# Kernel tuning notes

Hardware: AMD Instinct MI355X
Metric: run time of the kernel (lower is better)

## Reference

```python
import jax, jax.numpy as jnp
import numpy as np

N_NODES = 50000   # field_size == number of graph nodes
N_EDGES = 800000  # avg degree 16
VOCAB = 200000    # feature_size
EMB = 64          # embedding_size == in_dim
HID = 64          # num_hidden
SLOPE = 0.2       # leaky relu negative slope


def setup_inputs() -> dict:
    key = jax.random.key(0)
    ks = jax.random.split(key, 20)
    s = 0.05
    d = {}
    d["features"] = jax.random.randint(ks[0], (8, N_NODES), 0, VOCAB, dtype=jnp.int32)
    d["feature_values"] = jax.random.uniform(ks[1], (8, N_NODES), dtype=jnp.float32)
    d["src"] = jax.random.randint(ks[2], (N_EDGES,), 0, N_NODES, dtype=jnp.int32)
    d["dst"] = jax.random.randint(ks[3], (N_EDGES,), 0, N_NODES, dtype=jnp.int32)
    d["emb"] = jax.random.normal(ks[4], (VOCAB, EMB), jnp.float32) * s
    # layer 0: in=64 -> heads=2, out=64 (no residual)
    d["W0"]  = jax.random.normal(ks[5], (EMB, 2 * HID), jnp.float32) * s
    d["al0"] = jax.random.normal(ks[6], (2, HID), jnp.float32) * s
    d["ar0"] = jax.random.normal(ks[7], (2, HID), jnp.float32) * s
    d["b0"]  = jnp.zeros((2 * HID,), jnp.float32)
    # layer 1: in=128 -> heads=2, out=64 (identity residual since in == heads*out)
    d["W1"]  = jax.random.normal(ks[8], (2 * HID, 2 * HID), jnp.float32) * s
    d["al1"] = jax.random.normal(ks[9], (2, HID), jnp.float32) * s
    d["ar1"] = jax.random.normal(ks[10], (2, HID), jnp.float32) * s
    d["b1"]  = jnp.zeros((2 * HID,), jnp.float32)
    # output layer: in=128 -> heads=1, out=64 (projected residual), no activation
    d["W2"]    = jax.random.normal(ks[11], (2 * HID, EMB), jnp.float32) * s
    d["al2"]   = jax.random.normal(ks[12], (1, EMB), jnp.float32) * s
    d["ar2"]   = jax.random.normal(ks[13], (1, EMB), jnp.float32) * s
    d["b2"]    = jnp.zeros((EMB,), jnp.float32)
    d["resW2"] = jax.random.normal(ks[14], (2 * HID, EMB), jnp.float32) * s
    return d


def _gat_layer(h, src, dst, W, al, ar, b, res, act):
    """DGL-style GATConv. h: [N, in], W: [in, H*D], al/ar: [H, D]."""
    N = h.shape[0]
    H, D = al.shape
    fh = (h @ W).reshape(N, H, D)                      # [N, H, D]
    el = jnp.einsum('nhd,hd->nh', fh, al)              # [N, H]
    er = jnp.einsum('nhd,hd->nh', fh, ar)              # [N, H]
    e = jax.nn.leaky_relu(el[src] + er[dst], SLOPE)    # [E, H]
    # edge softmax grouped by destination node
    m = jax.ops.segment_max(e, dst, num_segments=N)
    m = jnp.where(jnp.isfinite(m), m, 0.0)
    ex = jnp.exp(e - m[dst])
    den = jax.ops.segment_sum(ex, dst, num_segments=N)
    alpha = ex / jnp.maximum(den[dst], 1e-9)           # [E, H]
    out = jax.ops.segment_sum(alpha[:, :, None] * fh[src], dst, num_segments=N)  # [N, H, D]
    if res is not None:
        out = out + res
    out = out + b.reshape(H, D)
    if act:
        out = jax.nn.elu(out)
    return out


def reference(features, feature_values, src, dst, emb,
              W0, al0, ar0, b0, W1, al1, ar1, b1,
              W2, al2, ar2, b2, resW2):
    # embedding lookup scaled by feature values: [B, field, emb]
    fe = emb[features] * feature_values[..., None]
    h = fe[0]                                          # [N_NODES, EMB]
    # layer 0: no residual, elu, flatten heads
    h = _gat_layer(h, src, dst, W0, al0, ar0, b0, None, True).reshape(N_NODES, -1)
    # layer 1: identity residual (in == heads*out), elu, flatten heads
    res1 = h.reshape(N_NODES, 2, HID)
    h = _gat_layer(h, src, dst, W1, al1, ar1, b1, res1, True).reshape(N_NODES, -1)
    # output layer: projected residual, no activation, mean over heads
    res2 = (h @ resW2).reshape(N_NODES, 1, EMB)
    logits = _gat_layer(h, src, dst, W2, al2, ar2, b2, res2, False).mean(axis=1)
    return logits
```

## Files before the change

kernel.cpp:

```cpp
#include <hip/hip_runtime.h>


typedef __attribute__((ext_vector_type(8))) short short8;
typedef __attribute__((ext_vector_type(4))) float float4v;

__device__ __forceinline__ float lrelu(float x){ return x >= 0.f ? x : 0.2f*x; }

__device__ __forceinline__ unsigned short f2bf(float f){
  unsigned int u = __float_as_uint(f);
  u += 0x7fffu + ((u >> 16) & 1u);
  return (unsigned short)(u >> 16);
}
__device__ __forceinline__ float bf2f(unsigned short u){
  return __uint_as_float((unsigned int)u << 16);
}
__device__ __forceinline__ float rl_f(float v, int l){
  return __int_as_float(__builtin_amdgcn_readlane(__float_as_int(v), l));
}

__global__ void k_zero_i32(int* __restrict__ p, int n){
  int i = blockIdx.x*blockDim.x + threadIdx.x;
  if (i < n) p[i] = 0;
}

__global__ void k_hist(const int* __restrict__ dst, int* __restrict__ counts, int E){
  int i = blockIdx.x*blockDim.x + threadIdx.x;
  if (i < E) atomicAdd(&counts[dst[i]], 1);
}

__global__ void k_scan_local(const int* __restrict__ counts, int* __restrict__ row_ptr,
                             int* __restrict__ bsum, int N){
  __shared__ int s[256];
  int t = threadIdx.x, g = blockIdx.x*256 + t;
  int v = (g < N) ? counts[g] : 0;
  s[t] = v; __syncthreads();
  #pragma unroll
  for (int off = 1; off < 256; off <<= 1){
    int x = 0;
    if (t >= off) x = s[t-off];
    __syncthreads();
    s[t] += x;
    __syncthreads();
  }
  if (g < N) row_ptr[g+1] = s[t];
  if (g == 0 && t == 0) row_ptr[0] = 0;
  if (t == 255) bsum[blockIdx.x] = s[255];
}

__global__ void k_scan_top(int* __restrict__ bsum, int nb){
  __shared__ int s[256];
  int t = threadIdx.x;
  int v = (t < nb) ? bsum[t] : 0;
  s[t] = v; __syncthreads();
  #pragma unroll
  for (int off = 1; off < 256; off <<= 1){
    int x = 0;
    if (t >= off) x = s[t-off];
    __syncthreads();
    s[t] += x;
    __syncthreads();
  }
  if (t < nb) bsum[t] = s[t] - v;
}

__global__ void k_scan_fix(int* __restrict__ row_ptr, const int* __restrict__ bsum, int N){
  int g = blockIdx.x*256 + threadIdx.x;
  if (g < N && blockIdx.x > 0) row_ptr[g+1] += bsum[blockIdx.x];
}

__global__ void k_scatter(const int* __restrict__ src, const int* __restrict__ dst,
                          const int* __restrict__ row_ptr, int* __restrict__ cursor,
                          int* __restrict__ ssrc, int E){
  int i = blockIdx.x*blockDim.x + threadIdx.x;
  if (i >= E) return;
  int d = dst[i];
  int pos = atomicAdd(&cursor[d], 1);
  ssrc[row_ptr[d] + pos] = src[i];
}

__global__ void k_wprep(const float* __restrict__ Wa, const float* __restrict__ Wb,
                        int IN, unsigned short* __restrict__ Wt){
  int id = blockIdx.x*256 + threadIdx.x;
  if (id >= 128*IN) return;
  int n = id / IN, k = id % IN;
  float v;
  if (Wb) v = (n < 64) ? Wa[k*64 + n] : Wb[k*64 + (n - 64)];
  else    v = Wa[k*128 + n];
  Wt[n*IN + k] = f2bf(v);
}

__global__ void k_embed(const int* __restrict__ feat, const float* __restrict__ fv,
                        const float* __restrict__ emb, unsigned int* __restrict__ h0b, int N){
  int t = blockIdx.x*blockDim.x + threadIdx.x;
  int n = t >> 4, c4 = t & 15;
  if (n >= N) return;
  float4 v = ((const float4*)(emb + (size_t)feat[n]*64))[c4];
  float sc = fv[n];
  unsigned int p0 = (unsigned)f2bf(v.x*sc) | ((unsigned)f2bf(v.y*sc) << 16);
  unsigned int p1 = (unsigned)f2bf(v.z*sc) | ((unsigned)f2bf(v.w*sc) << 16);
  h0b[(size_t)n*32 + c4*2]     = p0;
  h0b[(size_t)n*32 + c4*2 + 1] = p1;
}

template<int IN, int H>
__global__ __launch_bounds__(256) void k_gemm_mfma(
    const unsigned short* __restrict__ hb,
    const unsigned short* __restrict__ Wt,
    const float* __restrict__ al, const float* __restrict__ ar,
    unsigned short* __restrict__ fhb,
    float* __restrict__ elr, int N){
  constexpr int KS = IN/32;
  constexpr int LDP = IN + 8;
  __shared__ unsigned short Wt_s[128*LDP];
  const int t = threadIdx.x;
  const int lane = t & 63, wid = t >> 6;
  const int l15 = lane & 15, quad = lane >> 4;
  const int row0 = blockIdx.x*64 + wid*16;

  for (int id = t; id < 128*(IN/8); id += 256){
    int r = id/(IN/8), seg = id%(IN/8);
    ((uint4*)(Wt_s + r*LDP))[seg] = ((const uint4*)(Wt + (size_t)r*IN))[seg];
  }
  short8 a[KS];
  int arow = row0 + l15;
  #pragma unroll
  for (int s = 0; s < KS; s++){
    if (arow < N) a[s] = *(const short8*)(hb + (size_t)arow*IN + s*32 + quad*8);
    else          a[s] = short8{0,0,0,0,0,0,0,0};
  }
  __syncthreads();

  float4v acc[8];
  #pragma unroll
  for (int nt = 0; nt < 8; nt++) acc[nt] = float4v{0.f,0.f,0.f,0.f};
  #pragma unroll
  for (int nt = 0; nt < 8; nt++){
    #pragma unroll
    for (int s = 0; s < KS; s++){
      short8 b = *(const short8*)(Wt_s + (nt*16 + l15)*LDP + s*32 + quad*8);
      acc[nt] = __builtin_amdgcn_mfma_f32_16x16x32_bf16(a[s], b, acc[nt], 0, 0, 0);
    }
  }

  float alc[8], arc[8];
  #pragma unroll
  for (int nt = 0; nt < 8; nt++){
    bool hv = (H == 2) || (nt < 4);
    alc[nt] = hv ? al[nt*16 + l15] : 0.f;
    arc[nt] = hv ? ar[nt*16 + l15] : 0.f;
  }
  #pragma unroll
  for (int reg = 0; reg < 4; reg++){
    int row = row0 + quad*4 + reg;
    bool rv = row < N;
    if (rv){
      #pragma unroll
      for (int nt = 0; nt < 8; nt++)
        fhb[(size_t)row*128 + nt*16 + l15] = f2bf(acc[nt][reg]);
    }
    float pel0 = 0.f, per0 = 0.f, pel1 = 0.f, per1 = 0.f;
    #pragma unroll
    for (int nt = 0; nt < 4; nt++){
      pel0 += acc[nt][reg]*alc[nt];     per0 += acc[nt][reg]*arc[nt];
      pel1 += acc[nt+4][reg]*alc[nt+4]; per1 += acc[nt+4][reg]*arc[nt+4];
    }
    #pragma unroll
    for (int off = 1; off < 16; off <<= 1){
      pel0 += __shfl_xor(pel0, off, 64);
      pel1 += __shfl_xor(pel1, off, 64);
      per0 += __shfl_xor(per0, off, 64);
      per1 += __shfl_xor(per1, off, 64);
    }
    if (l15 == 0 && rv){
      elr[row*4+0] = pel0;
      elr[row*4+1] = (H == 2) ? pel1 : 0.f;
      elr[row*4+2] = per0;
      elr[row*4+3] = (H == 2) ? per1 : 0.f;
    }
  }
}

template<int H>
__global__ __launch_bounds__(256) void k_agg(
    const unsigned* __restrict__ fhb, const float* __restrict__ elr,
    const int* __restrict__ row_ptr, const int* __restrict__ ssrc,
    const float* __restrict__ bias, const float* __restrict__ res,
    int act, int res_from_fh,
    float* __restrict__ out, int out_ld, unsigned* __restrict__ outb, int N){
  int lane = threadIdx.x & 63, wid = threadIdx.x >> 6;
  int n = blockIdx.x*4 + wid;
  if (n >= N) return;
  int beg = row_ptr[n], end = row_ptr[n+1];
  float er0 = elr[n*4+2];
  float er1 = (H == 2) ? elr[n*4+3] : 0.f;

  float x0 = 0.f, x1 = 0.f;
  {
    int i = beg + lane;
    if (i < end){
      int s = ssrc[i];
      float2 el = *(const float2*)(elr + s*4);
      x0 = __expf(fminf(lrelu(el.x + er0), 30.f));
      if (H == 2) x1 = __expf(fminf(lrelu(el.y + er1), 30.f));
    }
  }
  float d0 = x0, d1 = x1;
  for (int i = beg + lane + 64; i < end; i += 64){
    int s = ssrc[i];
    float2 el = *(const float2*)(elr + s*4);
    d0 += __expf(fminf(lrelu(el.x + er0), 30.f));
    if (H == 2) d1 += __expf(fminf(lrelu(el.y + er1), 30.f));
  }
  #pragma unroll
  for (int off = 32; off >= 1; off >>= 1){
    d0 += __shfl_xor(d0, off, 64);
    if (H == 2) d1 += __shfl_xor(d1, off, 64);
  }
  float rd0 = d0 > 0.f ? 1.f/d0 : 0.f;
  float rd1 = (H == 2 && d1 > 0.f) ? 1.f/d1 : 0.f;

  float ax = 0.f, ay = 0.f;
  for (int base = beg; base < end; base += 64){
    int i = base + lane;
    int s = 0; float a0 = 0.f, a1 = 0.f;
    if (i < end){
      s = ssrc[i];
      if (base == beg){
        a0 = x0 * rd0; if (H == 2) a1 = x1 * rd1;
      } else {
        float2 el = *(const float2*)(elr + s*4);
        a0 = __expf(fminf(lrelu(el.x + er0), 30.f)) * rd0;
        if (H == 2) a1 = __expf(fminf(lrelu(el.y + er1), 30.f)) * rd1;
      }
    }
    int cnt  = min(64, end - base);
    int cnt8 = (cnt + 7) & ~7;
    if (H == 2){
      for (int j0 = 0; j0 < cnt8; j0 += 8){
        unsigned w[8]; float aj[8];
        #pragma unroll
        for (int u = 0; u < 8; u++){
          int sj = __builtin_amdgcn_readlane(s, j0 + u);
          w[u] = fhb[(size_t)sj*64 + lane];
        }
        #pragma unroll
        for (int u = 0; u < 8; u++){
          float aj0 = rl_f(a0, j0 + u);
          float aj1 = rl_f(a1, j0 + u);
          aj[u] = (lane < 32) ? aj0 : aj1;
        }
        #pragma unroll
        for (int u = 0; u < 8; u++){
          ax += bf2f((unsigned short)(w[u] & 0xffffu)) * aj[u];
          ay += bf2f((unsigned short)(w[u] >> 16))     * aj[u];
        }
      }
    } else {
      const unsigned short* fh16 = (const unsigned short*)fhb;
      for (int j0 = 0; j0 < cnt8; j0 += 8){
        unsigned short w[8]; float aj[8];
        #pragma unroll
        for (int u = 0; u < 8; u++){
          int sj = __builtin_amdgcn_readlane(s, j0 + u);
          w[u] = fh16[(size_t)sj*128 + lane];
        }
        #pragma unroll
        for (int u = 0; u < 8; u++) aj[u] = rl_f(a0, j0 + u);
        #pragma unroll
        for (int u = 0; u < 8; u++) ax += bf2f(w[u]) * aj[u];
      }
    }
  }
  if (H == 2){
    int c0 = lane*2;
    float o0 = ax + bias[c0], o1 = ay + bias[c0+1];
    if (res){ o0 += res[n*128 + c0]; o1 += res[n*128 + c0+1]; }
    if (act){ o0 = o0 > 0.f ? o0 : expm1f(o0); o1 = o1 > 0.f ? o1 : expm1f(o1); }
    *(float2*)(out + n*out_ld + c0) = make_float2(o0, o1);
    if (outb) outb[(size_t)n*64 + lane] = (unsigned)f2bf(o0) | ((unsigned)f2bf(o1) << 16);
  } else {
    const unsigned short* fh16 = (const unsigned short*)fhb;
    float o = ax + bias[lane];
    if (res_from_fh) o += bf2f(fh16[(size_t)n*128 + 64 + lane]);
    out[n*out_ld + lane] = o;
  }
}

extern "C" void kernel_launch(void* const* d_in, const int* in_sizes, int n_in,
                              void* d_out, int out_size, void* d_ws, size_t ws_size,
                              hipStream_t stream) {
  const int*   feat = (const int*)  d_in[0];
  const float* fv   = (const float*)d_in[1];
  const int*   src  = (const int*)  d_in[2];
  const int*   dst  = (const int*)  d_in[3];
  const float* emb  = (const float*)d_in[4];
  const float* W0   = (const float*)d_in[5];
  const float* al0  = (const float*)d_in[6];
  const float* ar0  = (const float*)d_in[7];
  const float* b0   = (const float*)d_in[8];
  const float* W1   = (const float*)d_in[9];
  const float* al1  = (const float*)d_in[10];
  const float* ar1  = (const float*)d_in[11];
  const float* b1   = (const float*)d_in[12];
  const float* W2   = (const float*)d_in[13];
  const float* al2  = (const float*)d_in[14];
  const float* ar2  = (const float*)d_in[15];
  const float* b2   = (const float*)d_in[16];
  const float* rW2  = (const float*)d_in[17];
  const int N = in_sizes[0] / 8;
  const int E = in_sizes[2];

  size_t off = 0;
  auto alloc = [&](size_t bytes) -> void* {
    void* p = (char*)d_ws + off;
    off = (off + bytes + 255) & ~(size_t)255;
    return p;
  };
  unsigned short* P1 = (unsigned short*)alloc((size_t)N*128*sizeof(unsigned short));
  float* P2     = (float*)alloc((size_t)N*128*sizeof(float));
  float* P3     = (float*)alloc((size_t)N*128*sizeof(float));
  unsigned short* hb = (unsigned short*)alloc((size_t)N*128*sizeof(unsigned short));
  float* elr    = (float*)alloc((size_t)N*4*sizeof(float));
  int* row_ptr  = (int*)alloc((size_t)(N+1)*sizeof(int));
  int* counts   = (int*)alloc((size_t)2*N*sizeof(int));
  int* cursor   = counts + N;
  int* ssrc     = (int*)alloc((size_t)E*sizeof(int));
  int* bsum     = (int*)alloc(256*sizeof(int));
  unsigned short* Wt0 = (unsigned short*)alloc((size_t)128*64*sizeof(unsigned short));
  unsigned short* Wt1 = (unsigned short*)alloc((size_t)128*128*sizeof(unsigned short));
  unsigned short* Wt2 = (unsigned short*)alloc((size_t)128*128*sizeof(unsigned short));

  int nb1 = (N + 255) / 256;
  k_zero_i32<<<(2*N + 255)/256, 256, 0, stream>>>(counts, 2*N);
  k_hist<<<(E + 255)/256, 256, 0, stream>>>(dst, counts, E);
  k_scan_local<<<nb1, 256, 0, stream>>>(counts, row_ptr, bsum, N);
  k_scan_top<<<1, 256, 0, stream>>>(bsum, nb1);
  k_scan_fix<<<nb1, 256, 0, stream>>>(row_ptr, bsum, N);
  k_scatter<<<(E + 255)/256, 256, 0, stream>>>(src, dst, row_ptr, cursor, ssrc, E);
  k_wprep<<<(128*64 + 255)/256, 256, 0, stream>>>(W0, nullptr, 64, Wt0);
  k_wprep<<<(128*128 + 255)/256, 256, 0, stream>>>(W1, nullptr, 128, Wt1);
  k_wprep<<<(128*128 + 255)/256, 256, 0, stream>>>(W2, rW2, 128, Wt2);
  k_embed<<<(N*16 + 255)/256, 256, 0, stream>>>(feat, fv, emb, (unsigned int*)hb, N);

  int gt = (N + 63)/64;
  int nagg = (N + 3)/4;
  k_gemm_mfma<64,2><<<gt, 256, 0, stream>>>(hb, Wt0, al0, ar0, P1, elr, N);
  k_agg<2><<<nagg, 256, 0, stream>>>((unsigned*)P1, elr, row_ptr, ssrc, b0, nullptr,
                                     1, 0, P2, 128, (unsigned*)hb, N);
  k_gemm_mfma<128,2><<<gt, 256, 0, stream>>>(hb, Wt1, al1, ar1, P1, elr, N);
  k_agg<2><<<nagg, 256, 0, stream>>>((unsigned*)P1, elr, row_ptr, ssrc, b1, P2,
                                     1, 0, P3, 128, (unsigned*)hb, N);
  k_gemm_mfma<128,1><<<gt, 256, 0, stream>>>(hb, Wt2, al2, ar2, P1, elr, N);
  k_agg<1><<<nagg, 256, 0, stream>>>((unsigned*)P1, elr, row_ptr, ssrc, b2, nullptr,
                                     0, 1, (float*)d_out, 64, nullptr, N);
}
```

Baseline: 367.4 us.

## Fuse embedding into first GEMM, merge weight prep, compress edge indices

Folds the embedding lookup and scaling into the first MFMA GEMM, so the bf16 h0 buffer is no longer written and read back. Merges the three weight-transpose launches into one kernel. Makes hist and scatter process 4 edges per thread, and stores sorted source indices as 16-bit to cut index traffic in aggregation. Raises the aggregation gather unroll from 8 to 16 for more loads in flight. The 16-bit indices only hold because N is 50000 (below 65536), so larger graphs would break.

```diff
diff --git a/kernel.cpp b/kernel.cpp
--- a/kernel.cpp
+++ b/kernel.cpp
@@ -24,8 +24,12 @@
 }
 
 __global__ void k_hist(const int* __restrict__ dst, int* __restrict__ counts, int E){
-  int i = blockIdx.x*blockDim.x + threadIdx.x;
-  if (i < E) atomicAdd(&counts[dst[i]], 1);
+  int i0 = (blockIdx.x*blockDim.x + threadIdx.x)*4;
+  #pragma unroll
+  for (int u = 0; u < 4; u++){
+    int i = i0 + u;
+    if (i < E) atomicAdd(&counts[dst[i]], 1);
+  }
 }
 
 __global__ void k_scan_local(const int* __restrict__ counts, int* __restrict__ row_ptr,
@@ -70,41 +74,41 @@
 
 __global__ void k_scatter(const int* __restrict__ src, const int* __restrict__ dst,
                           const int* __restrict__ row_ptr, int* __restrict__ cursor,
-                          int* __restrict__ ssrc, int E){
-  int i = blockIdx.x*blockDim.x + threadIdx.x;
-  if (i >= E) return;
-  int d = dst[i];
-  int pos = atomicAdd(&cursor[d], 1);
-  ssrc[row_ptr[d] + pos] = src[i];
-}
-
-__global__ void k_wprep(const float* __restrict__ Wa, const float* __restrict__ Wb,
-                        int IN, unsigned short* __restrict__ Wt){
+                          unsigned short* __restrict__ ssrc, int E){
+  int i0 = (blockIdx.x*blockDim.x + threadIdx.x)*4;
+  #pragma unroll
+  for (int u = 0; u < 4; u++){
+    int i = i0 + u;
+    if (i < E){
+      int d = dst[i];
+      int pos = atomicAdd(&cursor[d], 1);
+      ssrc[row_ptr[d] + pos] = (unsigned short)src[i];
+    }
+  }
+}
+
+__global__ void k_wprep_all(const float* __restrict__ W0, const float* __restrict__ W1,
+                            const float* __restrict__ W2, const float* __restrict__ rW2,
+                            unsigned short* __restrict__ Wt0, unsigned short* __restrict__ Wt1,
+                            unsigned short* __restrict__ Wt2){
   int id = blockIdx.x*256 + threadIdx.x;
-  if (id >= 128*IN) return;
-  int n = id / IN, k = id % IN;
-  float v;
-  if (Wb) v = (n < 64) ? Wa[k*64 + n] : Wb[k*64 + (n - 64)];
-  else    v = Wa[k*128 + n];
-  Wt[n*IN + k] = f2bf(v);
-}
-
-__global__ void k_embed(const int* __restrict__ feat, const float* __restrict__ fv,
-                        const float* __restrict__ emb, unsigned int* __restrict__ h0b, int N){
-  int t = blockIdx.x*blockDim.x + threadIdx.x;
-  int n = t >> 4, c4 = t & 15;
-  if (n >= N) return;
-  float4 v = ((const float4*)(emb + (size_t)feat[n]*64))[c4];
-  float sc = fv[n];
-  unsigned int p0 = (unsigned)f2bf(v.x*sc) | ((unsigned)f2bf(v.y*sc) << 16);
-  unsigned int p1 = (unsigned)f2bf(v.z*sc) | ((unsigned)f2bf(v.w*sc) << 16);
-  h0b[(size_t)n*32 + c4*2]     = p0;
-  h0b[(size_t)n*32 + c4*2 + 1] = p1;
-}
-
-template<int IN, int H>
+  if (id < 128*64){
+    int n = id/64, k = id%64;
+    Wt0[n*64 + k] = f2bf(W0[k*128 + n]);
+  } else if (id < 128*64 + 128*128){
+    int j = id - 128*64; int n = j/128, k = j%128;
+    Wt1[n*128 + k] = f2bf(W1[k*128 + n]);
+  } else if (id < 128*64 + 2*128*128){
+    int j = id - 128*64 - 128*128; int n = j/128, k = j%128;
+    float v = (n < 64) ? W2[k*64 + n] : rW2[k*64 + (n - 64)];
+    Wt2[n*128 + k] = f2bf(v);
+  }
+}
+
+template<int IN, int H, bool EMBED>
 __global__ __launch_bounds__(256) void k_gemm_mfma(
     const unsigned short* __restrict__ hb,
+    const int* __restrict__ feat, const float* __restrict__ fv, const float* __restrict__ emb,
     const unsigned short* __restrict__ Wt,
     const float* __restrict__ al, const float* __restrict__ ar,
     unsigned short* __restrict__ fhb,
@@ -123,10 +127,27 @@
   }
   short8 a[KS];
   int arow = row0 + l15;
-  #pragma unroll
-  for (int s = 0; s < KS; s++){
-    if (arow < N) a[s] = *(const short8*)(hb + (size_t)arow*IN + s*32 + quad*8);
-    else          a[s] = short8{0,0,0,0,0,0,0,0};
+  if (EMBED){
+    int f = 0; float sc = 0.f;
+    if (arow < N){ f = feat[arow]; sc = fv[arow]; }
+    #pragma unroll
+    for (int s = 0; s < KS; s++){
+      const float* ep = emb + (size_t)f*64 + s*32 + quad*8;
+      float4 v0 = ((const float4*)ep)[0];
+      float4 v1 = ((const float4*)ep)[1];
+      short8 av;
+      av[0]=(short)f2bf(v0.x*sc); av[1]=(short)f2bf(v0.y*sc);
+      av[2]=(short)f2bf(v0.z*sc); av[3]=(short)f2bf(v0.w*sc);
+      av[4]=(short)f2bf(v1.x*sc); av[5]=(short)f2bf(v1.y*sc);
+      av[6]=(short)f2bf(v1.z*sc); av[7]=(short)f2bf(v1.w*sc);
+      a[s] = av;
+    }
+  } else {
+    #pragma unroll
+    for (int s = 0; s < KS; s++){
+      if (arow < N) a[s] = *(const short8*)(hb + (size_t)arow*IN + s*32 + quad*8);
+      else          a[s] = short8{0,0,0,0,0,0,0,0};
+    }
   }
   __syncthreads();
 
@@ -183,7 +204,7 @@
 template<int H>
 __global__ __launch_bounds__(256) void k_agg(
     const unsigned* __restrict__ fhb, const float* __restrict__ elr,
-    const int* __restrict__ row_ptr, const int* __restrict__ ssrc,
+    const int* __restrict__ row_ptr, const unsigned short* __restrict__ ssrc,
     const float* __restrict__ bias, const float* __restrict__ res,
     int act, int res_from_fh,
     float* __restrict__ out, int out_ld, unsigned* __restrict__ outb, int N){
@@ -233,41 +254,41 @@
         if (H == 2) a1 = __expf(fminf(lrelu(el.y + er1), 30.f)) * rd1;
       }
     }
-    int cnt  = min(64, end - base);
-    int cnt8 = (cnt + 7) & ~7;
+    int cnt   = min(64, end - base);
+    int cnt16 = (cnt + 15) & ~15;
     if (H == 2){
-      for (int j0 = 0; j0 < cnt8; j0 += 8){
-        unsigned w[8]; float aj[8];
-        #pragma unroll
-        for (int u = 0; u < 8; u++){
+      for (int j0 = 0; j0 < cnt16; j0 += 16){
+        unsigned w[16]; float aj[16];
+        #pragma unroll
+        for (int u = 0; u < 16; u++){
           int sj = __builtin_amdgcn_readlane(s, j0 + u);
           w[u] = fhb[(size_t)sj*64 + lane];
         }
         #pragma unroll
-        for (int u = 0; u < 8; u++){
+        for (int u = 0; u < 16; u++){
           float aj0 = rl_f(a0, j0 + u);
           float aj1 = rl_f(a1, j0 + u);
           aj[u] = (lane < 32) ? aj0 : aj1;
         }
         #pragma unroll
-        for (int u = 0; u < 8; u++){
+        for (int u = 0; u < 16; u++){
           ax += bf2f((unsigned short)(w[u] & 0xffffu)) * aj[u];
           ay += bf2f((unsigned short)(w[u] >> 16))     * aj[u];
         }
       }
     } else {
       const unsigned short* fh16 = (const unsigned short*)fhb;
-      for (int j0 = 0; j0 < cnt8; j0 += 8){
-        unsigned short w[8]; float aj[8];
-        #pragma unroll
-        for (int u = 0; u < 8; u++){
+      for (int j0 = 0; j0 < cnt16; j0 += 16){
+        unsigned short w[16]; float aj[16];
+        #pragma unroll
+        for (int u = 0; u < 16; u++){
           int sj = __builtin_amdgcn_readlane(s, j0 + u);
           w[u] = fh16[(size_t)sj*128 + lane];
         }
         #pragma unroll
-        for (int u = 0; u < 8; u++) aj[u] = rl_f(a0, j0 + u);
-        #pragma unroll
-        for (int u = 0; u < 8; u++) ax += bf2f(w[u]) * aj[u];
+        for (int u = 0; u < 16; u++) aj[u] = rl_f(a0, j0 + u);
+        #pragma unroll
+        for (int u = 0; u < 16; u++) ax += bf2f(w[u]) * aj[u];
       }
     }
   }
@@ -324,7 +345,7 @@
   int* row_ptr  = (int*)alloc((size_t)(N+1)*sizeof(int));
   int* counts   = (int*)alloc((size_t)2*N*sizeof(int));
   int* cursor   = counts + N;
-  int* ssrc     = (int*)alloc((size_t)E*sizeof(int));
+  unsigned short* ssrc = (unsigned short*)alloc((size_t)E*sizeof(unsigned short));
   int* bsum     = (int*)alloc(256*sizeof(int));
   unsigned short* Wt0 = (unsigned short*)alloc((size_t)128*64*sizeof(unsigned short));
   unsigned short* Wt1 = (unsigned short*)alloc((size_t)128*128*sizeof(unsigned short));
@@ -332,25 +353,26 @@
 
   int nb1 = (N + 255) / 256;
   k_zero_i32<<<(2*N + 255)/256, 256, 0, stream>>>(counts, 2*N);
-  k_hist<<<(E + 255)/256, 256, 0, stream>>>(dst, counts, E);
+  k_hist<<<(E/4 + 255)/256, 256, 0, stream>>>(dst, counts, E);
   k_scan_local<<<nb1, 256, 0, stream>>>(counts, row_ptr, bsum, N);
   k_scan_top<<<1, 256, 0, stream>>>(bsum, nb1);
   k_scan_fix<<<nb1, 256, 0, stream>>>(row_ptr, bsum, N);
-  k_scatter<<<(E + 255)/256, 256, 0, stream>>>(src, dst, row_ptr, cursor, ssrc, E);
-  k_wprep<<<(128*64 + 255)/256, 256, 0, stream>>>(W0, nullptr, 64, Wt0);
-  k_wprep<<<(128*128 + 255)/256, 256, 0, stream>>>(W1, nullptr, 128, Wt1);
-  k_wprep<<<(128*128 + 255)/256, 256, 0, stream>>>(W2, rW2, 128, Wt2);
-  k_embed<<<(N*16 + 255)/256, 256, 0, stream>>>(feat, fv, emb, (unsigned int*)hb, N);
+  k_scatter<<<(E/4 + 255)/256, 256, 0, stream>>>(src, dst, row_ptr, cursor, ssrc, E);
+  k_wprep_all<<<(128*64 + 2*128*128 + 255)/256, 256, 0, stream>>>(
+      W0, W1, W2, rW2, Wt0, Wt1, Wt2);
 
   int gt = (N + 63)/64;
   int nagg = (N + 3)/4;
-  k_gemm_mfma<64,2><<<gt, 256, 0, stream>>>(hb, Wt0, al0, ar0, P1, elr, N);
+  k_gemm_mfma<64,2,true><<<gt, 256, 0, stream>>>(nullptr, feat, fv, emb,
+      Wt0, al0, ar0, P1, elr, N);
   k_agg<2><<<nagg, 256, 0, stream>>>((unsigned*)P1, elr, row_ptr, ssrc, b0, nullptr,
                                      1, 0, P2, 128, (unsigned*)hb, N);
-  k_gemm_mfma<128,2><<<gt, 256, 0, stream>>>(hb, Wt1, al1, ar1, P1, elr, N);
+  k_gemm_mfma<128,2,false><<<gt, 256, 0, stream>>>(hb, nullptr, nullptr, nullptr,
+      Wt1, al1, ar1, P1, elr, N);
   k_agg<2><<<nagg, 256, 0, stream>>>((unsigned*)P1, elr, row_ptr, ssrc, b1, P2,
                                      1, 0, P3, 128, (unsigned*)hb, N);
-  k_gemm_mfma<128,1><<<gt, 256, 0, stream>>>(hb, Wt2, al2, ar2, P1, elr, N);
+  k_gemm_mfma<128,1,false><<<gt, 256, 0, stream>>>(hb, nullptr, nullptr, nullptr,
+      Wt2, al2, ar2, P1, elr, N);
   k_agg<1><<<nagg, 256, 0, stream>>>((unsigned*)P1, elr, row_ptr, ssrc, b2, nullptr,
                                      0, 1, (float*)d_out, 64, nullptr, N);
 }
```

Result: slower. 378.2 us (+3.0%).
